# Performance work log

Measured on AMD Instinct MI355X. Metric: run time of the kernel, lower is better.

Reference implementation:

```python
import jax, jax.numpy as jnp
import numpy as np

TEMPERATURE = 0.07
EPS = 1e-12


def setup_inputs() -> dict:
    key = jax.random.key(0)
    k1, k2 = jax.random.split(key)
    B, D, C = 8192, 512, 100
    features = jax.random.normal(k1, (B, D), dtype=jnp.float32)
    labels = jax.random.randint(k2, (B,), 0, C, dtype=jnp.int64)
    return {"features": features, "labels": labels}


def reference(features, labels):
    B = features.shape[0]
    # L2-normalize features along feature dim
    f = features / jnp.linalg.norm(features, axis=1, keepdims=True)
    # positive-pair mask (same label), excluding self
    same = (labels[:, None] == labels[None, :]).astype(f.dtype)
    logits_mask = 1.0 - jnp.eye(B, dtype=f.dtype)
    mask = same * logits_mask
    # scaled cosine similarity logits, row-max subtracted for stability
    sim = jnp.matmul(f, f.T) / TEMPERATURE                      # [B, B]
    logits = sim - jax.lax.stop_gradient(sim.max(axis=1, keepdims=True))
    exp_logits = jnp.exp(logits) * logits_mask
    log_prob = logits - jnp.log(exp_logits.sum(axis=1, keepdims=True) + EPS)
    mask_sum = mask.sum(axis=1)                                  # [B]
    valid = (mask_sum > 0).astype(f.dtype)
    mean_log_prob_pos = (mask * log_prob).sum(axis=1) / (mask_sum + EPS)
    n_valid = valid.sum()
    loss = -jnp.sum(mean_log_prob_pos * valid) / jnp.maximum(n_valid, 1.0)
    return loss
```

## Files before the change

### kernel.cpp

```cpp
#include <hip/hip_runtime.h>
#include <hip/hip_bf16.h>

using short8 = __attribute__((ext_vector_type(8))) short;
using f32x4  = __attribute__((ext_vector_type(4))) float;
typedef long long i64f;
typedef unsigned char uchar;

constexpr int BSZ = 8192;
constexpr int DD  = 512;
constexpr int NC  = 100;
constexpr int NT  = 64;
constexpr int NBLK = NT * (NT + 1) / 2;
constexpr float INV_T = 1.0f / 0.07f;


static __device__ __forceinline__ void gload16(const void* g, void* l) {
    __builtin_amdgcn_global_load_lds((const __attribute__((address_space(1))) void*)g,
                                     (__attribute__((address_space(3))) void*)l, 16, 0, 0);
}

#define DSR64(dst, addr, imm) \
    asm volatile("ds_read_b64 %0, %1 offset:%2" : "=v"(dst) : "v"(addr), "i"(imm));

#define DPPADD(v, ctrl) { \
    int _x = __builtin_amdgcn_update_dpp(0, __float_as_int(v), ctrl, 0xf, 0xf, true); \
    v += __int_as_float(_x); }
#define ROWSUM16(v) { DPPADD(v, 0x128) DPPADD(v, 0x124) DPPADD(v, 0x122) DPPADD(v, 0x121) }

__global__ __launch_bounds__(256) void norm_rows(const float* __restrict__ feat,
                                                 uchar* __restrict__ fnrm8) {
    const int row = blockIdx.x * 4 + (threadIdx.x >> 6);
    const int l   = threadIdx.x & 63;
    const float4* src = reinterpret_cast<const float4*>(feat + (size_t)row * DD);
    float4 v0 = src[l * 2 + 0];
    float4 v1 = src[l * 2 + 1];
    float ss = v0.x*v0.x + v0.y*v0.y + v0.z*v0.z + v0.w*v0.w
             + v1.x*v1.x + v1.y*v1.y + v1.z*v1.z + v1.w*v1.w;
    #pragma unroll
    for (int m = 32; m >= 1; m >>= 1) ss += __shfl_xor(ss, m, 64);
    const float rn = rsqrtf(ss);
    int w0 = __builtin_amdgcn_cvt_pk_fp8_f32(v0.x * rn, v0.y * rn, 0,  false);
    w0     = __builtin_amdgcn_cvt_pk_fp8_f32(v0.z * rn, v0.w * rn, w0, true);
    int w1 = __builtin_amdgcn_cvt_pk_fp8_f32(v1.x * rn, v1.y * rn, 0,  false);
    w1     = __builtin_amdgcn_cvt_pk_fp8_f32(v1.z * rn, v1.w * rn, w1, true);
    uint2 q; q.x = (unsigned)w0; q.y = (unsigned)w1;
    const int off = ((l >> 2) << 5) + ((((l & 3) ^ ((row >> 2) & 3))) << 3);
    *reinterpret_cast<uint2*>(fnrm8 + (size_t)row * DD + off) = q;
}

__global__ __launch_bounds__(256) void gsum(const uchar* __restrict__ fnrm8,
                                            const int* __restrict__ labels,
                                            float* __restrict__ cls_val,
                                            int* __restrict__ counts) {
    __shared__ int   slab[BSZ];
    __shared__ float gred[4][DD];
    __shared__ float sq4[4];
    __shared__ int   cc[4];

    const int t = threadIdx.x, w = t >> 6, lam = t & 63;
    for (int i = t; i < BSZ; i += 256) slab[i] = labels[i];
    __syncthreads();

    const int c = blockIdx.x;
    float a[8] = {0.f,0.f,0.f,0.f,0.f,0.f,0.f,0.f};
    int cnt = 0;
    const int kt_off = (lam >> 2) << 5;
    for (int base = w * 2048; base < (w + 1) * 2048; base += 64) {
        const unsigned long long m0 = __ballot(slab[base + lam] == c);
        cnt += (int)__popcll(m0);
        unsigned long long m = m0;
        while (m) {
            const int j = __ffsll((long long)m) - 1; m &= m - 1;
            const int r = base + j;
            const int off = kt_off + ((((lam & 3) ^ ((r >> 2) & 3))) << 3);
            const uint2 q = *reinterpret_cast<const uint2*>(
                fnrm8 + (size_t)r * DD + off);
            a[0] += __builtin_amdgcn_cvt_f32_fp8(q.x, 0);
            a[1] += __builtin_amdgcn_cvt_f32_fp8(q.x, 1);
            a[2] += __builtin_amdgcn_cvt_f32_fp8(q.x, 2);
            a[3] += __builtin_amdgcn_cvt_f32_fp8(q.x, 3);
            a[4] += __builtin_amdgcn_cvt_f32_fp8(q.y, 0);
            a[5] += __builtin_amdgcn_cvt_f32_fp8(q.y, 1);
            a[6] += __builtin_amdgcn_cvt_f32_fp8(q.y, 2);
            a[7] += __builtin_amdgcn_cvt_f32_fp8(q.y, 3);
        }
    }
    #pragma unroll
    for (int d = 0; d < 8; ++d) gred[w][lam * 8 + d] = a[d];
    if (lam == 0) cc[w] = cnt;
    __syncthreads();

    const float g0 = gred[0][t] + gred[1][t] + gred[2][t] + gred[3][t];
    const float g1 = gred[0][t + 256] + gred[1][t + 256] + gred[2][t + 256] + gred[3][t + 256];
    float sq = g0 * g0 + g1 * g1;
    #pragma unroll
    for (int m = 32; m >= 1; m >>= 1) sq += __shfl_xor(sq, m, 64);
    if (lam == 0) sq4[w] = sq;
    __syncthreads();
    if (t == 0) {
        const float gsq = sq4[0] + sq4[1] + sq4[2] + sq4[3];
        const int   n   = cc[0] + cc[1] + cc[2] + cc[3];
        counts[c]  = n;
        cls_val[c] = (n >= 2) ? (gsq - (float)n) * INV_T / (float)(n - 1) : 0.f;
    }
}

__global__ __launch_bounds__(256, 4) void supcon_main(const uchar* __restrict__ fnrm8,
                                                      float* __restrict__ part_denom) {
    __shared__ __align__(16) uchar smem[3 * 8192];

    const int raw = blockIdx.x;
    const int bid = (raw & 7) * 260 + (raw >> 3);
    int rt = 0, rem = bid;
    while (rem >= NT - rt) { rem -= NT - rt; ++rt; }
    const int ct = rt + rem;
    const bool diag = (ct == rt);

    const int t  = threadIdx.x;
    const int l  = t & 63;
    const int lr = l & 15, grp = l >> 4;
    const int w  = t >> 6;
    const int wr = w >> 1, wc = w & 1;
    const int rowBase = rt * 128, colBase = ct * 128;

    const int srow = t >> 1;
    const uchar* g8A = fnrm8 + (size_t)(rowBase + srow) * DD + (t & 1) * 16;
    const uchar* g8B = fnrm8 + (size_t)(colBase + srow) * DD + (t & 1) * 16;
    uchar* S = smem;
    const int t16 = t * 16;

    #define STG(kt, b) { \
        gload16(g8A + (kt) * 32, S + (b) * 8192 +        t16); \
        gload16(g8B + (kt) * 32, S + (b) * 8192 + 4096 + t16); }

    const int slot = grp ^ ((lr >> 2) & 3);
    const int va = (wr * 64 + lr) * 32 + slot * 8;
    const int vb = 4096 + (wc * 64 + lr) * 32 + slot * 8;

    f32x4 acc[4][4];
    #pragma unroll
    for (int i = 0; i < 4; ++i)
        #pragma unroll
        for (int j = 0; j < 4; ++j) acc[i][j] = f32x4{0.f, 0.f, 0.f, 0.f};

    STG(0, 0)
    STG(1, 1)

    #pragma unroll
    for (int it = 0; it < 16; ++it) {
        const int b = it % 3;
        if (it < 15) { asm volatile("s_waitcnt vmcnt(2)" ::: "memory"); }
        else         { asm volatile("s_waitcnt vmcnt(0)" ::: "memory"); }
        __builtin_amdgcn_s_barrier();
        if (it < 14) {
            const int nb = (it + 2) % 3;
            STG(it + 2, nb)
        }

        i64f aF[4], bF[4];
        DSR64(aF[0], va, (b * 8192) + 0)     DSR64(aF[1], va, (b * 8192) + 512)
        DSR64(aF[2], va, (b * 8192) + 1024)  DSR64(aF[3], va, (b * 8192) + 1536)
        DSR64(bF[0], vb, (b * 8192) + 0)     DSR64(bF[1], vb, (b * 8192) + 512)
        DSR64(bF[2], vb, (b * 8192) + 1024)  DSR64(bF[3], vb, (b * 8192) + 1536)
        asm volatile("s_waitcnt lgkmcnt(0)");
        __builtin_amdgcn_sched_barrier(0);
        __builtin_amdgcn_s_setprio(1);
        #pragma unroll
        for (int fa = 0; fa < 4; ++fa)
            #pragma unroll
            for (int fb = 0; fb < 4; ++fb)
                acc[fa][fb] = __builtin_amdgcn_mfma_f32_16x16x32_fp8_fp8(
                    aF[fa], bF[fb], acc[fa][fb], 0, 0, 0);
        __builtin_amdgcn_s_setprio(0);
    }
    #undef STG

    __syncthreads();
    float* red  = reinterpret_cast<float*>(smem);
    float* cred = reinterpret_cast<float*>(smem) + 256;

    float cdv[4] = {0.f, 0.f, 0.f, 0.f};
    #pragma unroll
    for (int fa = 0; fa < 4; ++fa) {
        #pragma unroll
        for (int r = 0; r < 4; ++r) {
            const int row_l = wr * 64 + fa * 16 + grp * 4 + r;
            const int grow  = rowBase + row_l;
            float dsum = 0.f;
            #pragma unroll
            for (int fb = 0; fb < 4; ++fb) {
                const int col_l = wc * 64 + fb * 16 + lr;
                const float e  = __expf(acc[fa][fb][r] * INV_T - INV_T);
                const float ev = ((colBase + col_l) != grow) ? e : 0.f;
                dsum += ev; cdv[fb] += ev;
            }
            ROWSUM16(dsum)
            if (lr == 0) red[row_l * 2 + wc] = dsum;
        }
    }
    #pragma unroll
    for (int fb = 0; fb < 4; ++fb) {
        cdv[fb] += __shfl_xor(cdv[fb], 16, 64);
        cdv[fb] += __shfl_xor(cdv[fb], 32, 64);
    }
    if (grp == 0) {
        #pragma unroll
        for (int fb = 0; fb < 4; ++fb)
            cred[(wc * 64 + fb * 16 + lr) * 2 + wr] = cdv[fb];
    }
    __syncthreads();
    if (t < 128) {
        const float d = red[t * 2] + red[t * 2 + 1];
        part_denom[(size_t)ct * BSZ + rowBase + t] = d;
    } else if (!diag) {
        const int c = t - 128;
        const float d = cred[c * 2] + cred[c * 2 + 1];
        part_denom[(size_t)rt * BSZ + colBase + c] = d;
    }
}

__global__ __launch_bounds__(256) void row_finalize(const float* __restrict__ part_denom,
                                                    const int* __restrict__ counts,
                                                    const int* __restrict__ labels,
                                                    float* __restrict__ bsum,
                                                    float* __restrict__ bval) {
    __shared__ float s4[4], v4[4];
    const int t = threadIdx.x;
    const int row = blockIdx.x * 256 + t;
    float denom = 0.f;
    for (int k = 0; k < NT; ++k) denom += part_denom[(size_t)k * BSZ + row];
    const bool valid = counts[labels[row]] >= 2;
    float s = valid ? (INV_T + logf(denom + 1e-12f)) : 0.f;
    float v = valid ? 1.f : 0.f;
    #pragma unroll
    for (int m = 32; m >= 1; m >>= 1) { s += __shfl_xor(s, m, 64); v += __shfl_xor(v, m, 64); }
    if ((t & 63) == 0) { s4[t >> 6] = s; v4[t >> 6] = v; }
    __syncthreads();
    if (t == 0) {
        bsum[blockIdx.x] = s4[0] + s4[1] + s4[2] + s4[3];
        bval[blockIdx.x] = v4[0] + v4[1] + v4[2] + v4[3];
    }
}

__global__ __launch_bounds__(128) void final_reduce(const float* __restrict__ bsum,
                                                    const float* __restrict__ bval,
                                                    const float* __restrict__ cls_val,
                                                    float* __restrict__ out) {
    __shared__ float r2[2], q2[2], p2[2];
    const int t = threadIdx.x;
    float s = (t < 32) ? bsum[t] : 0.f;
    float v = (t < 32) ? bval[t] : 0.f;
    float p = (t < NC) ? cls_val[t] : 0.f;
    #pragma unroll
    for (int m = 32; m >= 1; m >>= 1) {
        s += __shfl_xor(s, m, 64); v += __shfl_xor(v, m, 64); p += __shfl_xor(p, m, 64);
    }
    if ((t & 63) == 0) { r2[t >> 6] = s; q2[t >> 6] = v; p2[t >> 6] = p; }
    __syncthreads();
    if (t == 0) {
        const float S = r2[0] + r2[1], V = q2[0] + q2[1], SP = p2[0] + p2[1];
        out[0] = -(SP - S) / fmaxf(V, 1.f);
    }
}

extern "C" void kernel_launch(void* const* d_in, const int* in_sizes, int n_in,
                              void* d_out, int out_size, void* d_ws, size_t ws_size,
                              hipStream_t stream) {
    const float* feat   = (const float*)d_in[0];
    const int*   labels = (const int*)d_in[1];
    float*       out    = (float*)d_out;

    char* ws = (char*)d_ws;
    uchar*  fnrm8      = (uchar*)ws;   ws += (size_t)BSZ * DD;
    float*  part_denom = (float*)ws;   ws += (size_t)NT * BSZ * 4;
    float*  cls_val    = (float*)ws;   ws += NC * 4 + 288;
    int*    counts     = (int*)ws;     ws += NC * 4 + 288;
    float*  bsum       = (float*)ws;   ws += 32 * 4;
    float*  bval       = (float*)ws;   ws += 32 * 4;

    hipLaunchKernelGGL(norm_rows,    dim3(BSZ / 4), dim3(256),  0, stream, feat, fnrm8);
    hipLaunchKernelGGL(gsum,         dim3(NC),      dim3(256),  0, stream,
                       fnrm8, labels, cls_val, counts);
    hipLaunchKernelGGL(supcon_main,  dim3(NBLK),    dim3(256),  0, stream,
                       fnrm8, part_denom);
    hipLaunchKernelGGL(row_finalize, dim3(BSZ/256), dim3(256),  0, stream,
                       part_denom, counts, labels, bsum, bval);
    hipLaunchKernelGGL(final_reduce, dim3(1),       dim3(128),  0, stream,
                       bsum, bval, cls_val, out);
}
```

Before: 68.89 us.

## Switch fp8 GEMM mainloop to 64-wide K tiles with double buffering

Replaces the triple-buffered 32-byte K-step pipeline (16 iterations) with a double-buffered pipeline that stages 64-byte K chunks (8 iterations), each consumed in two MFMA sub-steps. This halves the number of barriers and waitcnt points per tile and issues larger batched global-to-LDS loads. In exchange, prefetch depth drops to one stage and each iteration waits for vmcnt(0), so load latency may be less hidden. LDS use grows from 24KB to 32KB per block, which could affect occupancy at 4 blocks per CU.

```diff
diff --git a/kernel.cpp b/kernel.cpp
--- a/kernel.cpp
+++ b/kernel.cpp
@@ -1,7 +1,6 @@
 #include <hip/hip_runtime.h>
 #include <hip/hip_bf16.h>
 
-using short8 = __attribute__((ext_vector_type(8))) short;
 using f32x4  = __attribute__((ext_vector_type(4))) float;
 typedef long long i64f;
 typedef unsigned char uchar;
@@ -107,7 +106,7 @@
 
 __global__ __launch_bounds__(256, 4) void supcon_main(const uchar* __restrict__ fnrm8,
                                                       float* __restrict__ part_denom) {
-    __shared__ __align__(16) uchar smem[3 * 8192];
+    __shared__ __align__(16) uchar smem[2 * 16384];
 
     const int raw = blockIdx.x;
     const int bid = (raw & 7) * 260 + (raw >> 3);
@@ -123,19 +122,25 @@
     const int wr = w >> 1, wc = w & 1;
     const int rowBase = rt * 128, colBase = ct * 128;
 
-    const int srow = t >> 1;
-    const uchar* g8A = fnrm8 + (size_t)(rowBase + srow) * DD + (t & 1) * 16;
-    const uchar* g8B = fnrm8 + (size_t)(colBase + srow) * DD + (t & 1) * 16;
+    const int srow = t >> 2;
+    const uchar* g8A = fnrm8 + (size_t)(rowBase + srow) * DD + (t & 3) * 16;
+    const uchar* g8B = fnrm8 + (size_t)(colBase + srow) * DD + (t & 3) * 16;
     uchar* S = smem;
     const int t16 = t * 16;
 
     #define STG(kt, b) { \
-        gload16(g8A + (kt) * 32, S + (b) * 8192 +        t16); \
-        gload16(g8B + (kt) * 32, S + (b) * 8192 + 4096 + t16); }
+        gload16(g8A + (kt) * 64,           S + (b) * 16384 +         t16); \
+        gload16(g8A + (kt) * 64 + 64 * DD, S + (b) * 16384 +  4096 + t16); \
+        gload16(g8B + (kt) * 64,           S + (b) * 16384 +  8192 + t16); \
+        gload16(g8B + (kt) * 64 + 64 * DD, S + (b) * 16384 + 12288 + t16); }
 
     const int slot = grp ^ ((lr >> 2) & 3);
-    const int va = (wr * 64 + lr) * 32 + slot * 8;
-    const int vb = 4096 + (wc * 64 + lr) * 32 + slot * 8;
+    int va[2], vb[2];
+    #pragma unroll
+    for (int ks = 0; ks < 2; ++ks) {
+        va[ks] = (wr * 64 + lr) * 64 + ks * 32 + slot * 8;
+        vb[ks] = 8192 + (wc * 64 + lr) * 64 + ks * 32 + slot * 8;
+    }
 
     f32x4 acc[4][4];
     #pragma unroll
@@ -144,34 +149,32 @@
         for (int j = 0; j < 4; ++j) acc[i][j] = f32x4{0.f, 0.f, 0.f, 0.f};
 
     STG(0, 0)
-    STG(1, 1)
-
-    #pragma unroll
-    for (int it = 0; it < 16; ++it) {
-        const int b = it % 3;
-        if (it < 15) { asm volatile("s_waitcnt vmcnt(2)" ::: "memory"); }
-        else         { asm volatile("s_waitcnt vmcnt(0)" ::: "memory"); }
+
+    #pragma unroll
+    for (int it = 0; it < 8; ++it) {
+        const int b = it & 1;
+        asm volatile("s_waitcnt vmcnt(0)" ::: "memory");
         __builtin_amdgcn_s_barrier();
-        if (it < 14) {
-            const int nb = (it + 2) % 3;
-            STG(it + 2, nb)
+        if (it < 7) STG(it + 1, b ^ 1)
+
+        #pragma unroll
+        for (int ks = 0; ks < 2; ++ks) {
+            i64f aF[4], bF[4];
+            DSR64(aF[0], va[ks], (b * 16384) + 0)     DSR64(aF[1], va[ks], (b * 16384) + 1024)
+            DSR64(aF[2], va[ks], (b * 16384) + 2048)  DSR64(aF[3], va[ks], (b * 16384) + 3072)
+            DSR64(bF[0], vb[ks], (b * 16384) + 0)     DSR64(bF[1], vb[ks], (b * 16384) + 1024)
+            DSR64(bF[2], vb[ks], (b * 16384) + 2048)  DSR64(bF[3], vb[ks], (b * 16384) + 3072)
+            asm volatile("s_waitcnt lgkmcnt(0)");
+            __builtin_amdgcn_sched_barrier(0);
+            __builtin_amdgcn_s_setprio(1);
+            #pragma unroll
+            for (int fa = 0; fa < 4; ++fa)
+                #pragma unroll
+                for (int fb = 0; fb < 4; ++fb)
+                    acc[fa][fb] = __builtin_amdgcn_mfma_f32_16x16x32_fp8_fp8(
+                        aF[fa], bF[fb], acc[fa][fb], 0, 0, 0);
+            __builtin_amdgcn_s_setprio(0);
         }
-
-        i64f aF[4], bF[4];
-        DSR64(aF[0], va, (b * 8192) + 0)     DSR64(aF[1], va, (b * 8192) + 512)
-        DSR64(aF[2], va, (b * 8192) + 1024)  DSR64(aF[3], va, (b * 8192) + 1536)
-        DSR64(bF[0], vb, (b * 8192) + 0)     DSR64(bF[1], vb, (b * 8192) + 512)
-        DSR64(bF[2], vb, (b * 8192) + 1024)  DSR64(bF[3], vb, (b * 8192) + 1536)
-        asm volatile("s_waitcnt lgkmcnt(0)");
-        __builtin_amdgcn_sched_barrier(0);
-        __builtin_amdgcn_s_setprio(1);
-        #pragma unroll
-        for (int fa = 0; fa < 4; ++fa)
-            #pragma unroll
-            for (int fb = 0; fb < 4; ++fb)
-                acc[fa][fb] = __builtin_amdgcn_mfma_f32_16x16x32_fp8_fp8(
-                    aF[fa], bF[fb], acc[fa][fb], 0, 0, 0);
-        __builtin_amdgcn_s_setprio(0);
     }
     #undef STG
 
```

Result: faster. 61.06 us (median of 2 runs) (-11.4%).
